# Kernel tuning notes

Measured on AMD Instinct MI355X. Metric: run time of the kernel, lower is better.

Reference implementation:

```python
import jax, jax.numpy as jnp
import numpy as np

B = 2048          # batch
T = 64            # time_steps
H = 1024          # hidden_size
IN_FEATURES = T * H
WEIGHT_BITS = 8
INPUT_BITS = 8
CLIP_INIT = 2.5


def _fake_quant_ste(x, clip, bits):
    """Symmetric uniform fake quantization with straight-through rounding.

    clamp(x, -c, c), quantize to 2^(bits-1)-1 levels per side, dequantize.
    """
    n = float(2 ** (bits - 1) - 1)
    c = jnp.abs(clip)
    xc = jnp.clip(x, -c, c)
    scale = c / n
    q = jnp.round(xc / scale) * scale
    # straight-through estimator: forward = q, backward = d/dx clamp
    return xc + jax.lax.stop_gradient(q - xc)


def setup_inputs() -> dict:
    key = jax.random.key(0)
    k1, k2 = jax.random.split(key, 2)
    hidden_states = jax.random.normal(k1, (B, T, H), dtype=jnp.float32)
    # Linear(in=T*H, out=1) parameters
    weight = jax.random.normal(k2, (1, IN_FEATURES), dtype=jnp.float32) * 0.02
    bias = jnp.zeros((1,), dtype=jnp.float32)
    clip_val = jnp.asarray(CLIP_INIT, dtype=jnp.float32)  # learnable activation clip
    return {"hidden_states": hidden_states, "weight": weight,
            "bias": bias, "clip_val": clip_val}


def reference(hidden_states, weight, bias, clip_val):
    # nn.Flatten(): [B, T, H] -> [B, T*H]
    x = hidden_states.reshape(hidden_states.shape[0], -1)
    # input fake-quant with learnable layerwise clip
    xq = _fake_quant_ste(x, clip_val, INPUT_BITS)
    # weight fake-quant, layerwise scale from max |w| (scale treated as constant)
    w_clip = jax.lax.stop_gradient(jnp.max(jnp.abs(weight)))
    wq = _fake_quant_ste(weight, w_clip, WEIGHT_BITS)
    # GEMV-style linear (out_features = 1) + bias + tanh head
    out = xq @ wq.T + bias            # [B, 1]
    return jnp.tanh(out)
```

## Files before the change

kernel.cpp:

```cpp
#include <hip/hip_runtime.h>
#include <cmath>

static constexpr int BATCH = 2048;
static constexpr int K = 64 * 1024;
static constexpr int K4 = K / 4;

typedef float f4 __attribute__((ext_vector_type(4)));

__global__ __launch_bounds__(256)
void wmax_kernel(const float* __restrict__ w, unsigned int* __restrict__ wmax_bits) {
    const int tid = blockIdx.x * 256 + threadIdx.x;
    const f4* w4 = reinterpret_cast<const f4*>(w);
    float m = 0.0f;
#pragma unroll
    for (int r = 0; r < 2; ++r) {
        f4 v = w4[tid + r * 8192];
        m = fmaxf(m, fmaxf(fmaxf(fabsf(v.x), fabsf(v.y)),
                           fmaxf(fabsf(v.z), fabsf(v.w))));
    }
#pragma unroll
    for (int off = 32; off > 0; off >>= 1)
        m = fmaxf(m, __shfl_down(m, off, 64));
    if ((threadIdx.x & 63) == 0)
        atomicMax(wmax_bits, __float_as_uint(m));
}

__global__ __launch_bounds__(256)
void gemv_quant_tanh_kernel(const float* __restrict__ x,
                            const float* __restrict__ w,
                            const float* __restrict__ bias,
                            const float* __restrict__ clip,
                            const unsigned int* __restrict__ wmax_bits,
                            float* __restrict__ out) {
    const int row = blockIdx.x;
    const int tid = threadIdx.x;

    const float cx = fabsf(clip[0]);
    const float sx = cx * (1.0f / 127.0f);
    const float ix = 127.0f / cx;
    const float cw = __uint_as_float(wmax_bits[0]);
    const float sw = cw * (1.0f / 127.0f);
    const float iw = 127.0f / cw;

    const f4* xr = reinterpret_cast<const f4*>(x + (size_t)row * K);
    const f4* w4 = reinterpret_cast<const f4*>(w);

    float acc = 0.0f;
#pragma unroll 4
    for (int i = tid; i < K4; i += 256) {
        f4 xv = __builtin_nontemporal_load(&xr[i]);
        f4 wv = w4[i];
        float qx0 = rintf(fminf(fmaxf(xv.x, -cx), cx) * ix);
        float qx1 = rintf(fminf(fmaxf(xv.y, -cx), cx) * ix);
        float qx2 = rintf(fminf(fmaxf(xv.z, -cx), cx) * ix);
        float qx3 = rintf(fminf(fmaxf(xv.w, -cx), cx) * ix);
        float qw0 = rintf(wv.x * iw);
        float qw1 = rintf(wv.y * iw);
        float qw2 = rintf(wv.z * iw);
        float qw3 = rintf(wv.w * iw);
        acc = fmaf(qx0, qw0, acc);
        acc = fmaf(qx1, qw1, acc);
        acc = fmaf(qx2, qw2, acc);
        acc = fmaf(qx3, qw3, acc);
    }

#pragma unroll
    for (int off = 32; off > 0; off >>= 1)
        acc += __shfl_down(acc, off, 64);
    __shared__ float sm[4];
    if ((tid & 63) == 0) sm[tid >> 6] = acc;
    __syncthreads();
    if (tid == 0) {
        float s = (sm[0] + sm[1]) + (sm[2] + sm[3]);
        out[row] = tanhf(fmaf(s, sx * sw, bias[0]));
    }
}

extern "C" void kernel_launch(void* const* d_in, const int* in_sizes, int n_in,
                              void* d_out, int out_size, void* d_ws, size_t ws_size,
                              hipStream_t stream) {
    const float* x    = (const float*)d_in[0];
    const float* w    = (const float*)d_in[1];
    const float* bias = (const float*)d_in[2];
    const float* clip = (const float*)d_in[3];
    float* out = (float*)d_out;
    unsigned int* wmax_bits = (unsigned int*)d_ws;

    (void)hipMemsetAsync(wmax_bits, 0, sizeof(unsigned int), stream);
    wmax_kernel<<<32, 256, 0, stream>>>(w, wmax_bits);
    gemv_quant_tanh_kernel<<<BATCH, 256, 0, stream>>>(x, w, bias, clip, wmax_bits, out);
}
```

Measured before the change: 102.3 us.

## Pre-quantize weights to packed int8 and batch x loads in GEMV

```diff
diff --git a/kernel.cpp b/kernel.cpp
--- a/kernel.cpp
+++ b/kernel.cpp
@@ -7,8 +7,112 @@
 
 typedef float f4 __attribute__((ext_vector_type(4)));
 
+static constexpr size_t WS_NEEDED = 256 + (size_t)K;
+
 __global__ __launch_bounds__(256)
-void wmax_kernel(const float* __restrict__ w, unsigned int* __restrict__ wmax_bits) {
+void wmax_part_kernel(const float* __restrict__ w, float* __restrict__ wpart) {
+    const int tid = blockIdx.x * 256 + threadIdx.x;
+    const f4* w4 = reinterpret_cast<const f4*>(w);
+    float m = 0.0f;
+#pragma unroll
+    for (int r = 0; r < 2; ++r) {
+        f4 v = w4[tid + r * 8192];
+        m = fmaxf(m, fmaxf(fmaxf(fabsf(v.x), fabsf(v.y)),
+                           fmaxf(fabsf(v.z), fabsf(v.w))));
+    }
+#pragma unroll
+    for (int off = 32; off > 0; off >>= 1)
+        m = fmaxf(m, __shfl_down(m, off, 64));
+    __shared__ float sm[4];
+    if ((threadIdx.x & 63) == 0) sm[threadIdx.x >> 6] = m;
+    __syncthreads();
+    if (threadIdx.x == 0)
+        wpart[blockIdx.x] = fmaxf(fmaxf(sm[0], sm[1]), fmaxf(sm[2], sm[3]));
+}
+
+__global__ __launch_bounds__(256)
+void wquant_kernel(const float* __restrict__ w, const float* __restrict__ wpart,
+                   unsigned int* __restrict__ qw) {
+    float cw = 0.0f;
+#pragma unroll
+    for (int i = 0; i < 32; ++i) cw = fmaxf(cw, wpart[i]);
+    const float iw = 127.0f / cw;
+    const int t = blockIdx.x * 256 + threadIdx.x;
+    const f4* w4 = reinterpret_cast<const f4*>(w);
+#pragma unroll
+    for (int r = 0; r < 4; ++r) {
+        int idx = t + r * 4096;
+        f4 v = w4[idx];
+        int q0 = (int)rintf(v.x * iw), q1 = (int)rintf(v.y * iw);
+        int q2 = (int)rintf(v.z * iw), q3 = (int)rintf(v.w * iw);
+        qw[idx] = (unsigned int)((q0 & 0xff) | ((q1 & 0xff) << 8) |
+                                 ((q2 & 0xff) << 16) | ((q3 & 0xff) << 24));
+    }
+}
+
+__global__ __launch_bounds__(256)
+void gemv_quant_tanh_kernel(const float* __restrict__ x,
+                            const unsigned int* __restrict__ qw,
+                            const float* __restrict__ bias,
+                            const float* __restrict__ clip,
+                            const float* __restrict__ wpart,
+                            float* __restrict__ out) {
+    const int row = blockIdx.x;
+    const int tid = threadIdx.x;
+
+    float cw = 0.0f;
+#pragma unroll
+    for (int i = 0; i < 32; ++i) cw = fmaxf(cw, wpart[i]);
+    const float cx = fabsf(clip[0]);
+    const float ix = 127.0f / cx;
+    const float scale = (cx / 127.0f) * (cw / 127.0f);
+
+    const f4* xr = reinterpret_cast<const f4*>(x + (size_t)row * K);
+
+    float acc = 0.0f;
+    for (int outer = 0; outer < 8; ++outer) {
+        const int base = outer * 2048 + tid;
+        f4 xv[8];
+        unsigned int qv[8];
+#pragma unroll
+        for (int u = 0; u < 8; ++u)
+            xv[u] = __builtin_nontemporal_load(&xr[base + u * 256]);
+#pragma unroll
+        for (int u = 0; u < 8; ++u)
+            qv[u] = qw[base + u * 256];
+#pragma unroll
+        for (int u = 0; u < 8; ++u) {
+            f4 v = xv[u];
+            unsigned int q = qv[u];
+            float qx0 = rintf(__builtin_amdgcn_fmed3f(v.x, -cx, cx) * ix);
+            float qx1 = rintf(__builtin_amdgcn_fmed3f(v.y, -cx, cx) * ix);
+            float qx2 = rintf(__builtin_amdgcn_fmed3f(v.z, -cx, cx) * ix);
+            float qx3 = rintf(__builtin_amdgcn_fmed3f(v.w, -cx, cx) * ix);
+            float w0 = (float)((int)(q << 24) >> 24);
+            float w1 = (float)((int)(q << 16) >> 24);
+            float w2 = (float)((int)(q <<  8) >> 24);
+            float w3 = (float)((int)q >> 24);
+            acc = fmaf(qx0, w0, acc);
+            acc = fmaf(qx1, w1, acc);
+            acc = fmaf(qx2, w2, acc);
+            acc = fmaf(qx3, w3, acc);
+        }
+    }
+
+#pragma unroll
+    for (int off = 32; off > 0; off >>= 1)
+        acc += __shfl_down(acc, off, 64);
+    __shared__ float sm[4];
+    if ((tid & 63) == 0) sm[tid >> 6] = acc;
+    __syncthreads();
+    if (tid == 0) {
+        float s = (sm[0] + sm[1]) + (sm[2] + sm[3]);
+        out[row] = tanhf(fmaf(s, scale, bias[0]));
+    }
+}
+
+__global__ __launch_bounds__(256)
+void wmax_atomic_kernel(const float* __restrict__ w, unsigned int* __restrict__ wmax_bits) {
     const int tid = blockIdx.x * 256 + threadIdx.x;
     const f4* w4 = reinterpret_cast<const f4*>(w);
     float m = 0.0f;
@@ -26,44 +130,33 @@
 }
 
 __global__ __launch_bounds__(256)
-void gemv_quant_tanh_kernel(const float* __restrict__ x,
-                            const float* __restrict__ w,
-                            const float* __restrict__ bias,
-                            const float* __restrict__ clip,
-                            const unsigned int* __restrict__ wmax_bits,
-                            float* __restrict__ out) {
+void gemv_fallback_kernel(const float* __restrict__ x, const float* __restrict__ w,
+                          const float* __restrict__ bias, const float* __restrict__ clip,
+                          const unsigned int* __restrict__ wmax_bits,
+                          float* __restrict__ out) {
     const int row = blockIdx.x;
     const int tid = threadIdx.x;
-
     const float cx = fabsf(clip[0]);
-    const float sx = cx * (1.0f / 127.0f);
     const float ix = 127.0f / cx;
     const float cw = __uint_as_float(wmax_bits[0]);
-    const float sw = cw * (1.0f / 127.0f);
     const float iw = 127.0f / cw;
-
+    const float scale = (cx / 127.0f) * (cw / 127.0f);
     const f4* xr = reinterpret_cast<const f4*>(x + (size_t)row * K);
     const f4* w4 = reinterpret_cast<const f4*>(w);
-
     float acc = 0.0f;
 #pragma unroll 4
     for (int i = tid; i < K4; i += 256) {
         f4 xv = __builtin_nontemporal_load(&xr[i]);
         f4 wv = w4[i];
-        float qx0 = rintf(fminf(fmaxf(xv.x, -cx), cx) * ix);
-        float qx1 = rintf(fminf(fmaxf(xv.y, -cx), cx) * ix);
-        float qx2 = rintf(fminf(fmaxf(xv.z, -cx), cx) * ix);
-        float qx3 = rintf(fminf(fmaxf(xv.w, -cx), cx) * ix);
-        float qw0 = rintf(wv.x * iw);
-        float qw1 = rintf(wv.y * iw);
-        float qw2 = rintf(wv.z * iw);
-        float qw3 = rintf(wv.w * iw);
-        acc = fmaf(qx0, qw0, acc);
-        acc = fmaf(qx1, qw1, acc);
-        acc = fmaf(qx2, qw2, acc);
-        acc = fmaf(qx3, qw3, acc);
+        float qx0 = rintf(__builtin_amdgcn_fmed3f(xv.x, -cx, cx) * ix);
+        float qx1 = rintf(__builtin_amdgcn_fmed3f(xv.y, -cx, cx) * ix);
+        float qx2 = rintf(__builtin_amdgcn_fmed3f(xv.z, -cx, cx) * ix);
+        float qx3 = rintf(__builtin_amdgcn_fmed3f(xv.w, -cx, cx) * ix);
+        acc = fmaf(qx0, rintf(wv.x * iw), acc);
+        acc = fmaf(qx1, rintf(wv.y * iw), acc);
+        acc = fmaf(qx2, rintf(wv.z * iw), acc);
+        acc = fmaf(qx3, rintf(wv.w * iw), acc);
     }
-
 #pragma unroll
     for (int off = 32; off > 0; off >>= 1)
         acc += __shfl_down(acc, off, 64);
@@ -72,7 +165,7 @@
     __syncthreads();
     if (tid == 0) {
         float s = (sm[0] + sm[1]) + (sm[2] + sm[3]);
-        out[row] = tanhf(fmaf(s, sx * sw, bias[0]));
+        out[row] = tanhf(fmaf(s, scale, bias[0]));
     }
 }
 
@@ -84,9 +177,17 @@
     const float* bias = (const float*)d_in[2];
     const float* clip = (const float*)d_in[3];
     float* out = (float*)d_out;
-    unsigned int* wmax_bits = (unsigned int*)d_ws;
 
-    (void)hipMemsetAsync(wmax_bits, 0, sizeof(unsigned int), stream);
-    wmax_kernel<<<32, 256, 0, stream>>>(w, wmax_bits);
-    gemv_quant_tanh_kernel<<<BATCH, 256, 0, stream>>>(x, w, bias, clip, wmax_bits, out);
+    if (ws_size >= WS_NEEDED) {
+        float* wpart = (float*)d_ws;
+        unsigned int* qw = (unsigned int*)((char*)d_ws + 256);
+        wmax_part_kernel<<<32, 256, 0, stream>>>(w, wpart);
+        wquant_kernel<<<16, 256, 0, stream>>>(w, wpart, qw);
+        gemv_quant_tanh_kernel<<<BATCH, 256, 0, stream>>>(x, qw, bias, clip, wpart, out);
+    } else {
+        unsigned int* wmax_bits = (unsigned int*)d_ws;
+        (void)hipMemsetAsync(wmax_bits, 0, sizeof(unsigned int), stream);
+        wmax_atomic_kernel<<<32, 256, 0, stream>>>(w, wmax_bits);
+        gemv_fallback_kernel<<<BATCH, 256, 0, stream>>>(x, w, bias, clip, wmax_bits, out);
+    }
 }
```

Measured after the change: 86.40 us. -15.5%, faster.
